# Optimization experiments

Hardware: AMD Instinct MI355X
Metric: run time of the kernel (lower is better)

Reference implementation:

```python
import jax, jax.numpy as jnp
import numpy as np

N, F, H, K, E = 50000, 64, 64, 16, 800000
EXPONENT = 1.0  # module default; s = softmax(logits)**exponent, renormalized
EPS = 1e-15


def gcn_conv(x, W, b, src, dst, ew, n):
    """GCNConv: X' = D^{-1/2}(A+I)D^{-1/2} X W + b (symmetric norm, self-loops)."""
    h = x @ W  # [N,H] linear before propagation
    idx = jnp.arange(n)
    src_a = jnp.concatenate([src, idx])
    dst_a = jnp.concatenate([dst, idx])
    w_a = jnp.concatenate([ew, jnp.ones((n,), h.dtype)])
    deg = jax.ops.segment_sum(w_a, dst_a, num_segments=n)
    dinv = jnp.where(deg > 0, jax.lax.rsqrt(deg), 0.0)
    norm = dinv[src_a] * w_a * dinv[dst_a]          # [E+N]
    out = jax.ops.segment_sum(norm[:, None] * h[src_a], dst_a, num_segments=n)
    return out + b


def setup_inputs() -> dict:
    key = jax.random.key(0)
    ks = jax.random.split(key, 10)
    x = jax.random.normal(ks[0], (N, F), dtype=jnp.float32)
    edge_index = jax.random.randint(ks[1], (2, E), 0, N, dtype=jnp.int64)
    edge_weight = jax.random.uniform(ks[2], (E,), dtype=jnp.float32)
    W1 = jax.random.normal(ks[3], (F, H), dtype=jnp.float32) * (1.0 / np.sqrt(F))
    b1 = jnp.zeros((H,), jnp.float32)
    W2 = jax.random.normal(ks[4], (H, H), dtype=jnp.float32) * (1.0 / np.sqrt(H))
    b2 = jnp.zeros((H,), jnp.float32)
    Wp = jax.random.normal(ks[5], (H, K), dtype=jnp.float32) * (1.0 / np.sqrt(H))
    bp = jnp.zeros((K,), jnp.float32)
    return {"x": x, "edge_index": edge_index, "edge_weight": edge_weight,
            "W1": W1, "b1": b1, "W2": W2, "b2": b2, "Wp": Wp, "bp": bp}


def reference(x, edge_index, edge_weight, W1, b1, W2, b2, Wp, bp):
    src, dst = edge_index[0], edge_index[1]
    n = x.shape[0]
    k = Wp.shape[1]
    # stacked GCN + SELU
    h = jax.nn.selu(gcn_conv(x, W1, b1, src, dst, edge_weight, n))
    h = jax.nn.selu(gcn_conv(h, W2, b2, src, dst, edge_weight, n))
    # DMoN soft assignment
    s = jax.nn.softmax(h @ Wp + bp, axis=-1)          # [N,K]
    s = s ** EXPONENT
    s = s / s.sum(-1, keepdims=True)
    # pooled features: SELU(S^T X)
    out = jax.nn.selu(s.T @ h)                        # [K,H]
    # pooled adjacency: S^T A S computed over the edge list
    out_adj = jnp.einsum('ek,ec->kc', s[src] * edge_weight[:, None], s[dst])
    # spectral (modularity) loss
    d = jax.ops.segment_sum(edge_weight, src, num_segments=n)  # degrees
    two_m = edge_weight.sum()
    ca = s.T @ d                                      # [K]
    spectral_loss = -(jnp.trace(out_adj) - (ca @ ca) / two_m) / two_m
    # orthogonality loss
    ss = s.T @ s
    i_k = jnp.eye(k, dtype=s.dtype)
    ortho_loss = jnp.linalg.norm(ss / jnp.linalg.norm(ss) - i_k / jnp.sqrt(jnp.float32(k)))
    # cluster-size loss
    cluster_loss = jnp.linalg.norm(s.sum(0)) / n * jnp.sqrt(jnp.float32(k)) - 1.0
    # post-process pooled adjacency: zero diag, symmetric degree normalization
    adj = out_adj * (1.0 - i_k)
    dd = jnp.sqrt(adj.sum(-1))[:, None] + EPS
    adj = adj / dd / dd.T
    return s[None], out[None], adj[None], spectral_loss, ortho_loss, cluster_loss
```

## Files before the change

kernel.cpp:

```cpp
#include <hip/hip_runtime.h>
#include <hip/hip_bf16.h>

typedef __hip_bfloat16 bf16;
typedef long long i64t;

__device__ __forceinline__ float b2f(bf16 x) { return __bfloat162float(x); }
__device__ __forceinline__ bf16 f2b(float x) { return __float2bfloat16(x); }

__device__ __forceinline__ float loadF(const void* p, int isbf, long long i) {
    return isbf ? b2f(((const bf16*)p)[i]) : ((const float*)p)[i];
}
__device__ __forceinline__ int loadI(const void* p, int is64, long long i) {
    return is64 ? (int)((const i64t*)p)[i] : ((const int*)p)[i];
}
__device__ __forceinline__ void storeO(void* p, int isbf, long long i, float v) {
    if (isbf) ((bf16*)p)[i] = f2b(v);
    else ((float*)p)[i] = v;
}

#define SELU_ALPHA 1.6732632423543772f
#define SELU_SCALE 1.0507009873554805f
__device__ __forceinline__ float selu_f(float x) {
    return SELU_SCALE * (x > 0.f ? x : SELU_ALPHA * (expf(x) - 1.f));
}

__device__ __forceinline__ void atomAddF(float* p, float v) { unsafeAtomicAdd(p, v); }

__device__ __forceinline__ int pk_src(unsigned p) { return (int)(p >> 16); }
__device__ __forceinline__ float pk_w(unsigned p) { return __uint_as_float(p << 16); }

#define RED_STY 0
#define RED_OADJ 1024
#define RED_SS 1280
#define RED_CA 1536
#define RED_CS 1552
#define RED_2M 1568

#define NB_OADJ 1024
#define CH 2048
#define NBK 256
#define BW 256
#define CAP 4096
#define NRED 1568

__device__ float blockReduceSum256(float v) {
    __shared__ float part[4];
    for (int m = 32; m; m >>= 1) v += __shfl_down(v, m, 64);
    int wid = threadIdx.x >> 6, lane = threadIdx.x & 63;
    if (lane == 0) part[wid] = v;
    __syncthreads();
    v = part[0] + part[1] + part[2] + part[3];
    __syncthreads();
    return v;
}

__global__ void k_gemm_first(const void* __restrict__ in, const void* __restrict__ W,
                             int* __restrict__ zbase, int zcount,
                             bf16* __restrict__ out, int n) {
    __shared__ float Wl[4096];
    __shared__ float Rl[2048];
    __shared__ int scW[1];
    int t = threadIdx.x;
    int g = blockIdx.x * 256 + t;
    if (g < zcount) zbase[g] = 0;
    if (t == 0) scW[0] = 0;
    __syncthreads();
    {
        const unsigned* wq = (const unsigned*)W;
        int c0 = 0;
        for (int i = t; i < 2048; i += 256) {
            unsigned lo = wq[i] & 0xFFFFu, e = (lo >> 7) & 0xFFu;
            if (e == 0u || (e >= 0x60u && e <= 0x8Fu)) c0++;
        }
        atomicAdd(&scW[0], c0);
    }
    __syncthreads();
    int fb = scW[0] > 1200 ? 1 : 0;
    for (int idx = t; idx < 4096; idx += 256) Wl[idx] = loadF(W, fb, idx);
    int r0 = blockIdx.x * 32;
    for (int idx = t; idx < 2048; idx += 256) {
        int rl = idx >> 6, k = idx & 63;
        int r = r0 + rl;
        Rl[idx] = (r < n) ? loadF(in, fb, (long long)r * 64 + k) : 0.f;
    }
    __syncthreads();
    int rl = t >> 6, c = t & 63;
    float acc[8];
#pragma unroll
    for (int u = 0; u < 8; u++) acc[u] = 0.f;
    for (int k = 0; k < 64; k++) {
        float wv = Wl[k * 64 + c];
#pragma unroll
        for (int u = 0; u < 8; u++) acc[u] += Rl[(rl + (u << 2)) * 64 + k] * wv;
    }
#pragma unroll
    for (int u = 0; u < 8; u++) {
        int r = r0 + rl + (u << 2);
        if (r < n) out[(long long)r * 64 + c] = f2b(acc[u]);
    }
}

__global__ void k_bscatter(const void* __restrict__ W1, const void* __restrict__ eidx,
                           const void* __restrict__ ew, int* __restrict__ flags,
                           int* __restrict__ gofs, uint2* __restrict__ tmp, int E) {
    __shared__ int cnt[NBK];
    __shared__ int binStart[NBK];
    __shared__ int bofs[NBK];
    __shared__ int runBase[NBK];
    __shared__ int sc[NBK];
    __shared__ uint2 staged[CH];
    __shared__ int sc2[2];
    int t = threadIdx.x;
    cnt[t] = 0;
    if (t < 2) sc2[t] = 0;
    __syncthreads();
    const unsigned* wq = (const unsigned*)W1;
    int c0 = 0;
    for (int i = t; i < 2048; i += 256) {
        unsigned lo = wq[i] & 0xFFFFu;
        unsigned e = (lo >> 7) & 0xFFu;
        if (e == 0u || (e >= 0x60u && e <= 0x8Fu)) c0++;
    }
    const unsigned* iw = (const unsigned*)eidx;
    int c1 = 0;
    for (int i = t; i < 2048; i += 256)
        if (iw[2 * i + 1] == 0u) c1++;
    atomicAdd(&sc2[0], c0);
    atomicAdd(&sc2[1], c1);
    __syncthreads();
    int fb = sc2[0] > 1200 ? 1 : 0;
    int fi = sc2[1] > 1024 ? 1 : 0;
    if (blockIdx.x == 0 && t == 0) {
        flags[0] = fb;
        flags[1] = fi;
    }
    int base = blockIdx.x * CH;
    int m = min(CH, E - base);
    unsigned es[8], ed[8];
#pragma unroll
    for (int u = 0; u < 8; u++) {
        int k = t + u * 256;
        if (k < m) {
            int s = loadI(eidx, fi, base + k);
            int d = loadI(eidx, fi, (long long)E + base + k);
            float w = loadF(ew, fb, base + k);
            unsigned wb = (__float_as_uint(w) + 0x8000u) >> 16;
            es[u] = ((unsigned)s << 16) | wb;
            ed[u] = (unsigned)d;
            atomicAdd(&cnt[d >> 8], 1);
        } else {
            ed[u] = 0xFFFFFFFFu;
        }
    }
    __syncthreads();
    sc[t] = cnt[t];
    __syncthreads();
    for (int off = 1; off < NBK; off <<= 1) {
        int v = (t >= off) ? sc[t - off] : 0;
        __syncthreads();
        sc[t] += v;
        __syncthreads();
    }
    int ex = t ? sc[t - 1] : 0;
    binStart[t] = ex;
    bofs[t] = ex;
    __syncthreads();
#pragma unroll
    for (int u = 0; u < 8; u++) {
        if (ed[u] != 0xFFFFFFFFu) {
            int b = (int)(ed[u] >> 8);
            int li = atomicAdd(&bofs[b], 1);
            staged[li] = make_uint2(es[u], ed[u]);
        }
    }
    int c = cnt[t];
    __syncthreads();
    runBase[t] = c ? atomicAdd(&gofs[t], c) : 0;
    __syncthreads();
    for (int i = t; i < m; i += 256) {
        uint2 e = staged[i];
        int b = (int)(e.y >> 8);
        int rel = runBase[b] + (i - binStart[b]);
        if (rel < CAP) tmp[(long long)b * CAP + rel] = e;
    }
}

__global__ void k_build(const uint2* __restrict__ tmp, const int* __restrict__ gofs,
                        int* __restrict__ rowptr, int* __restrict__ rowend,
                        unsigned* __restrict__ srcW, float* __restrict__ dinv,
                        float* __restrict__ two_m, int n) {
    __shared__ int cnt[BW];
    __shared__ int nofs[BW];
    __shared__ float wsum[BW];
    __shared__ int inc[BW];
    int b = blockIdx.x;
    int t = threadIdx.x;
    int n0 = b << 8;
    int nn = min(BW, n - n0);
    cnt[t] = 0;
    wsum[t] = 0.f;
    __syncthreads();
    int lo = b * CAP;
    int hi = lo + min(gofs[b], CAP);
    for (int i = lo + t; i < hi; i += 256) {
        uint2 e = tmp[i];
        int dlo = (int)e.y - n0;
        atomicAdd(&cnt[dlo], 1);
        atomicAdd(&wsum[dlo], pk_w(e.x));
    }
    __syncthreads();
    inc[t] = cnt[t];
    __syncthreads();
    for (int off = 1; off < BW; off <<= 1) {
        int v = (t >= off) ? inc[t - off] : 0;
        __syncthreads();
        inc[t] += v;
        __syncthreads();
    }
    if (t < nn) {
        int ex = t ? inc[t - 1] : 0;
        rowptr[n0 + t] = lo + ex;
        rowend[n0 + t] = lo + inc[t];
        nofs[t] = lo + ex;
        dinv[n0 + t] = rsqrtf(wsum[t] + 1.f);
    }
    {
        float v = (t < nn) ? wsum[t] : 0.f;
        __shared__ float part[4];
        for (int mm = 32; mm; mm >>= 1) v += __shfl_down(v, mm, 64);
        int wid = t >> 6, lane = t & 63;
        if (lane == 0) part[wid] = v;
        __syncthreads();
        if (t == 0) atomAddF(two_m, part[0] + part[1] + part[2] + part[3]);
    }
    __syncthreads();
    for (int i = lo + t; i < hi; i += 256) {
        uint2 e = tmp[i];
        int dlo = (int)e.y - n0;
        int pos = atomicAdd(&nofs[dlo], 1);
        srcW[pos] = e.x;
    }
}

__global__ void k_gemm64(const void* __restrict__ in, const void* __restrict__ W,
                         const int* __restrict__ flags, bf16* __restrict__ out, int n) {
    __shared__ float Wl[4096];
    __shared__ float Rl[2048];
    int t = threadIdx.x;
    int fb = flags[0];
    for (int idx = t; idx < 4096; idx += 256) Wl[idx] = loadF(W, fb, idx);
    int r0 = blockIdx.x * 32;
    for (int idx = t; idx < 2048; idx += 256) {
        int rl = idx >> 6, k = idx & 63;
        int r = r0 + rl;
        Rl[idx] = (r < n) ? ((const float*)in)[(long long)r * 64 + k] : 0.f;
    }
    __syncthreads();
    int rl = t >> 6, c = t & 63;
    float acc[8];
#pragma unroll
    for (int u = 0; u < 8; u++) acc[u] = 0.f;
    for (int k = 0; k < 64; k++) {
        float wv = Wl[k * 64 + c];
#pragma unroll
        for (int u = 0; u < 8; u++) acc[u] += Rl[(rl + (u << 2)) * 64 + k] * wv;
    }
#pragma unroll
    for (int u = 0; u < 8; u++) {
        int r = r0 + rl + (u << 2);
        if (r < n) out[(long long)r * 64 + c] = f2b(acc[u]);
    }
}

__global__ void k_prop_csr(const int* __restrict__ rowptr, const int* __restrict__ rowend,
                           const unsigned* __restrict__ srcW, const float* __restrict__ dinv,
                           const bf16* __restrict__ hin, const void* __restrict__ b,
                           const int* __restrict__ flags, float* __restrict__ out, int n) {
    int t = threadIdx.x;
    int node = blockIdx.x * 4 + (t >> 6);
    if (node >= n) return;
    int l = t & 63;
    int q = l >> 4;
    int k = l & 15;
    int fb = flags[0];
    int i0 = rowptr[node], i1 = rowend[node];
    float di = dinv[node];
    float a0 = 0.f, a1 = 0.f, a2 = 0.f, a3 = 0.f;
    for (int base = i0; base < i1; base += 64) {
        int idx = base + l;
        unsigned p = (idx < i1) ? srcW[idx] : 0u;
        float cw = pk_w(p) * dinv[pk_src(p)];
        int m = i1 - base;
        if (m > 64) m = 64;
        for (int j = 0; j < m; j += 4) {
            unsigned pe = (unsigned)__shfl((int)p, j + q, 64);
            float c = __shfl(cw, j + q, 64);
            int s = (int)(pe >> 16);
            uint2 hv = *(const uint2*)(hin + ((long long)s << 6) + (k << 2));
            a0 += c * __uint_as_float(hv.x << 16);
            a1 += c * __uint_as_float(hv.x & 0xFFFF0000u);
            a2 += c * __uint_as_float(hv.y << 16);
            a3 += c * __uint_as_float(hv.y & 0xFFFF0000u);
        }
    }
    a0 += __shfl_xor(a0, 16, 64); a0 += __shfl_xor(a0, 32, 64);
    a1 += __shfl_xor(a1, 16, 64); a1 += __shfl_xor(a1, 32, 64);
    a2 += __shfl_xor(a2, 16, 64); a2 += __shfl_xor(a2, 32, 64);
    a3 += __shfl_xor(a3, 16, 64); a3 += __shfl_xor(a3, 32, 64);
    if (q == 0) {
        uint2 hv = *(const uint2*)(hin + ((long long)node << 6) + (k << 2));
        float dd = di * di;
        float v0 = di * a0 + dd * __uint_as_float(hv.x << 16) + loadF(b, fb, 4 * k);
        float v1 = di * a1 + dd * __uint_as_float(hv.x & 0xFFFF0000u) + loadF(b, fb, 4 * k + 1);
        float v2 = di * a2 + dd * __uint_as_float(hv.y << 16) + loadF(b, fb, 4 * k + 2);
        float v3 = di * a3 + dd * __uint_as_float(hv.y & 0xFFFF0000u) + loadF(b, fb, 4 * k + 3);
        float4 r = make_float4(selu_f(v0), selu_f(v1), selu_f(v2), selu_f(v3));
        *(float4*)(out + ((long long)node << 6) + (k << 2)) = r;
    }
}

__global__ void k_softmax(const float* __restrict__ y, const void* __restrict__ Wp,
                          const void* __restrict__ bp, const int* __restrict__ flags,
                          float* __restrict__ sbuf, void* __restrict__ sout,
                          float* __restrict__ scratch, int n) {
    __shared__ float Wl[1024];
    __shared__ float bl[16];
    __shared__ float yl[1024];
    __shared__ float sl[256];
    int t = threadIdx.x;
    int fb = flags[0];
    for (int idx = t; idx < 1024; idx += 256) Wl[idx] = loadF(Wp, fb, idx);
    if (t < 16) bl[t] = loadF(bp, fb, t);
    int g0 = blockIdx.x * 16;
    for (int idx = t; idx < 1024; idx += 256) {
        int nl = idx >> 6, f = idx & 63;
        int g = g0 + nl;
        yl[idx] = (g < n) ? y[(long long)g * 64 + f] : 0.f;
    }
    __syncthreads();
    int nl = t >> 4, k = t & 15;
    int g = g0 + nl;
    float logit = bl[k];
#pragma unroll
    for (int jj = 0; jj < 64; jj++) logit += yl[nl * 64 + jj] * Wl[jj * 16 + k];
    float mx = logit;
    for (int m = 8; m; m >>= 1) mx = fmaxf(mx, __shfl_xor(mx, m, 16));
    float e = expf(logit - mx);
    float sum = e;
    for (int m = 8; m; m >>= 1) sum += __shfl_xor(sum, m, 16);
    float sv = e / sum;
    sl[nl * 16 + k] = (g < n) ? sv : 0.f;
    if (g < n) {
        sbuf[(long long)g * 16 + k] = sv;
        storeO(sout, fb, (long long)g * 16 + k, sv);
    }
    __syncthreads();
    float* dst = scratch + (long long)blockIdx.x * 1280;
    {
        int k4 = t >> 6, f = t & 63;
        float a0 = 0.f, a1 = 0.f, a2 = 0.f, a3 = 0.f;
#pragma unroll
        for (int node = 0; node < 16; node++) {
            float yv = yl[node * 64 + f];
            const float* sp = sl + node * 16;
            a0 += sp[k4] * yv;
            a1 += sp[k4 + 4] * yv;
            a2 += sp[k4 + 8] * yv;
            a3 += sp[k4 + 12] * yv;
        }
        dst[k4 * 64 + f] = a0;
        dst[(k4 + 4) * 64 + f] = a1;
        dst[(k4 + 8) * 64 + f] = a2;
        dst[(k4 + 12) * 64 + f] = a3;
    }
    {
        int i = t >> 4, j = t & 15;
        float ssa = 0.f;
#pragma unroll
        for (int node = 0; node < 16; node++) ssa += sl[node * 16 + i] * sl[node * 16 + j];
        dst[1024 + t] = ssa;
    }
}

__global__ void k_outadj_csr(const int* __restrict__ rowptr, const int* __restrict__ rowend,
                             const unsigned* __restrict__ srcW, const float* __restrict__ s,
                             float* __restrict__ scratch, int n) {
    __shared__ float lacc[256];
    __shared__ float sca[16];
    __shared__ float scs[16];
    int t = threadIdx.x;
    int wv = t >> 6;
    int l = t & 63;
    int q = l >> 4;
    int j = l & 15;
    lacc[t] = 0.f;
    if (t < 16) { sca[t] = 0.f; scs[t] = 0.f; }
    __syncthreads();
    float acc[16];
#pragma unroll
    for (int r = 0; r < 16; r++) acc[r] = 0.f;
    float catot = 0.f, cstot = 0.f;
    for (int node = blockIdx.x * 4 + wv; node < n; node += NB_OADJ * 4) {
        int i0 = rowptr[node], i1 = rowend[node];
        float tv = 0.f;
        for (int base = i0; base < i1; base += 64) {
            int idx = base + l;
            unsigned p = (idx < i1) ? srcW[idx] : 0u;
            float wl = pk_w(p);
            int m = i1 - base;
            if (m > 64) m = 64;
            for (int jj = 0; jj < m; jj += 4) {
                unsigned pe = (unsigned)__shfl((int)p, jj + q, 64);
                float w = __shfl(wl, jj + q, 64);
                int sidx = (int)(pe >> 16);
                tv += w * s[(long long)sidx * 16 + j];
            }
        }
        tv += __shfl_xor(tv, 16, 64);
        tv += __shfl_xor(tv, 32, 64);
        float sj = s[(long long)node * 16 + j];
        if (q == 0) {
            catot += tv;
            cstot += sj;
        }
#pragma unroll
        for (int r = 0; r < 16; r++) acc[r] += __shfl(tv, r, 16) * sj;
    }
    if (q == 0) {
#pragma unroll
        for (int r = 0; r < 16; r++) atomicAdd(&lacc[r * 16 + j], acc[r]);
        atomicAdd(&sca[j], catot);
        atomicAdd(&scs[j], cstot);
    }
    __syncthreads();
    float* dstp = scratch + (long long)blockIdx.x * 288;
    dstp[t] = lacc[t];
    if (t < 16) {
        dstp[256 + t] = sca[t];
        dstp[272 + t] = scs[t];
    }
}

__global__ void k_reduce_fin(const float* __restrict__ sscr, const float* __restrict__ oscr,
                             float* __restrict__ red, int* __restrict__ done, int nbS,
                             void* __restrict__ out, const int* __restrict__ flags,
                             int n_nodes, int base) {
    int o = blockIdx.x;
    int t = threadIdx.x;
    float sum = 0.f;
    if (o < 1280) {
        for (int b = t; b < nbS; b += 256) sum += sscr[(long long)b * 1280 + o];
    } else {
        int oo = o - 1280;
        for (int b = t; b < NB_OADJ; b += 256) sum += oscr[(long long)b * 288 + oo];
    }
    float v = blockReduceSum256(sum);
    __shared__ int amLast;
    if (t == 0) {
        if (o < 1024) red[RED_STY + o] = v;
        else if (o < 1280) red[RED_SS + o - 1024] = v;
        else {
            int oo = o - 1280;
            if (oo < 256) red[RED_OADJ + oo] = v;
            else if (oo < 272) red[RED_CA + oo - 256] = v;
            else red[RED_CS + oo - 272] = v;
        }
        __threadfence();
        amLast = (atomicAdd(done, 1) == NRED - 1) ? 1 : 0;
    }
    __syncthreads();
    if (!amLast) return;
    __threadfence();
    int fb = flags[0];
    for (int idx = t; idx < 1024; idx += 256)
        storeO(out, fb, base + idx, selu_f(red[RED_STY + idx]));
    int i = t >> 4, j = t & 15;
    float ss_t = red[RED_SS + t];
    float oadj_t = red[RED_OADJ + t];
    float two_m = red[RED_2M];

    float norm_ss = sqrtf(blockReduceSum256(ss_t * ss_t));
    float diff = ss_t / norm_ss - ((i == j) ? 0.25f : 0.f);
    float ortho = sqrtf(blockReduceSum256(diff * diff));
    float trace = blockReduceSum256((i == j) ? oadj_t : 0.f);
    float ca_t = (t < 16) ? red[RED_CA + t] : 0.f;
    float cad = blockReduceSum256(ca_t * ca_t);
    float spectral = -(trace - cad / two_m) / two_m;
    float cs_t = (t < 16) ? red[RED_CS + t] : 0.f;
    float cluster = sqrtf(blockReduceSum256(cs_t * cs_t)) / (float)n_nodes * 4.f - 1.f;

    float a = (i == j) ? 0.f : oadj_t;
    float rs = a;
    for (int m = 8; m; m >>= 1) rs += __shfl_xor(rs, m, 16);
    __shared__ float ddl[16];
    float dd_i = sqrtf(rs) + 1e-15f;
    if (j == 0) ddl[i] = dd_i;
    __syncthreads();
    float aout = a / (dd_i * ddl[j]);
    storeO(out, fb, base + 1024 + t, aout);
    if (t == 0) {
        storeO(out, fb, base + 1280, spectral);
        storeO(out, fb, base + 1281, ortho);
        storeO(out, fb, base + 1282, cluster);
    }
}

extern "C" void kernel_launch(void* const* d_in, const int* in_sizes, int n_in,
                              void* d_out, int out_size, void* d_ws, size_t ws_size,
                              hipStream_t stream) {
    const void* x = d_in[0];
    const void* eidx = d_in[1];
    const void* ew = d_in[2];
    const void* W1 = d_in[3];
    const void* b1 = d_in[4];
    const void* W2 = d_in[5];
    const void* b2 = d_in[6];
    const void* Wp = d_in[7];
    const void* bp = d_in[8];

    const int N = in_sizes[0] / 64;
    const int E = in_sizes[2];

    float* ws = (float*)d_ws;
    float* B = ws;
    float* hbf_f = B + (size_t)N * 64;
    bf16* hbf = (bf16*)hbf_f;
    float* sbuf = hbf_f;
    float* dinv = hbf_f + (size_t)N * 32;
    int* rowptr = (int*)(dinv + N);
    int* rowend = rowptr + N;
    float* red = (float*)(rowend + N);
    int* gofs = (int*)(red + 2048);
    int* flags = gofs + NBK;
    int* done = flags + 2;
    size_t off_ints = (size_t)((done + 1) - (int*)ws);
    off_ints = (off_ints + 3) & ~(size_t)3;
    unsigned* srcW = (unsigned*)((int*)ws + off_ints);
    size_t off2 = off_ints + (size_t)NBK * CAP;
    off2 = (off2 + 3) & ~(size_t)3;
    uint2* tmp = (uint2*)((int*)ws + off2);
    float* sscr = (float*)tmp;
    int nbS = (N + 15) / 16;
    float* oscr = sscr + (size_t)nbS * 1280;

    int nbA = (E + CH - 1) / CH;
    int nbK = (N + BW - 1) / BW;
    int zcount = 2048 + NBK + 2 + 1;

    k_gemm_first<<<(N + 31) / 32, 256, 0, stream>>>(x, W1, (int*)red, zcount, hbf, N);
    k_bscatter<<<nbA, 256, 0, stream>>>(W1, eidx, ew, flags, gofs, tmp, E);
    k_build<<<nbK, 256, 0, stream>>>(tmp, gofs, rowptr, rowend, srcW, dinv,
                                     red + RED_2M, N);
    k_prop_csr<<<(N + 3) / 4, 256, 0, stream>>>(rowptr, rowend, srcW, dinv, hbf, b1,
                                                flags, B, N);
    k_gemm64<<<(N + 31) / 32, 256, 0, stream>>>(B, W2, flags, hbf, N);
    k_prop_csr<<<(N + 3) / 4, 256, 0, stream>>>(rowptr, rowend, srcW, dinv, hbf, b2,
                                                flags, B, N);
    k_softmax<<<nbS, 256, 0, stream>>>(B, Wp, bp, flags, sbuf, d_out, sscr, N);
    k_outadj_csr<<<NB_OADJ, 256, 0, stream>>>(rowptr, rowend, srcW, sbuf, oscr, N);
    k_reduce_fin<<<NRED, 256, 0, stream>>>(sscr, oscr, red, done, nbS, d_out, flags,
                                           N, N * 16);
}
```

Baseline: 356.0 us.

## Process 64 nodes per softmax block and split final reduction into separate kernel

The softmax kernel now loops over four 16-node tiles per block and accumulates S^T·H and S^T·S partials in registers. This cuts the number of partial-result slabs written to scratch and later summed by four. The last-block-done atomic counter in the reduction kernel is replaced by a separate single-block finalize launch, removing the threadfence/atomic path at the cost of one extra kernel launch. Fewer softmax blocks may reduce parallelism, and the extra syncs per tile add some latency.

```diff
diff --git a/kernel.cpp b/kernel.cpp
--- a/kernel.cpp
+++ b/kernel.cpp
@@ -41,7 +41,6 @@
 #define NBK 256
 #define BW 256
 #define CAP 4096
-#define NRED 1568
 
 __device__ float blockReduceSum256(float v) {
     __shared__ float part[4];
@@ -331,34 +330,34 @@
     int fb = flags[0];
     for (int idx = t; idx < 1024; idx += 256) Wl[idx] = loadF(Wp, fb, idx);
     if (t < 16) bl[t] = loadF(bp, fb, t);
-    int g0 = blockIdx.x * 16;
-    for (int idx = t; idx < 1024; idx += 256) {
-        int nl = idx >> 6, f = idx & 63;
-        int g = g0 + nl;
-        yl[idx] = (g < n) ? y[(long long)g * 64 + f] : 0.f;
-    }
-    __syncthreads();
-    int nl = t >> 4, k = t & 15;
-    int g = g0 + nl;
-    float logit = bl[k];
-#pragma unroll
-    for (int jj = 0; jj < 64; jj++) logit += yl[nl * 64 + jj] * Wl[jj * 16 + k];
-    float mx = logit;
-    for (int m = 8; m; m >>= 1) mx = fmaxf(mx, __shfl_xor(mx, m, 16));
-    float e = expf(logit - mx);
-    float sum = e;
-    for (int m = 8; m; m >>= 1) sum += __shfl_xor(sum, m, 16);
-    float sv = e / sum;
-    sl[nl * 16 + k] = (g < n) ? sv : 0.f;
-    if (g < n) {
-        sbuf[(long long)g * 16 + k] = sv;
-        storeO(sout, fb, (long long)g * 16 + k, sv);
-    }
-    __syncthreads();
-    float* dst = scratch + (long long)blockIdx.x * 1280;
-    {
-        int k4 = t >> 6, f = t & 63;
-        float a0 = 0.f, a1 = 0.f, a2 = 0.f, a3 = 0.f;
+    int k4 = t >> 6, f = t & 63;
+    int si = t >> 4, sj = t & 15;
+    float a0 = 0.f, a1 = 0.f, a2 = 0.f, a3 = 0.f, ssa = 0.f;
+    for (int it = 0; it < 4; it++) {
+        int g0 = (blockIdx.x * 4 + it) * 16;
+        __syncthreads();
+        for (int idx = t; idx < 1024; idx += 256) {
+            int nl = idx >> 6, ff = idx & 63;
+            int g = g0 + nl;
+            yl[idx] = (g < n) ? y[(long long)g * 64 + ff] : 0.f;
+        }
+        __syncthreads();
+        int g = g0 + si;
+        float logit = bl[sj];
+#pragma unroll
+        for (int jj = 0; jj < 64; jj++) logit += yl[si * 64 + jj] * Wl[jj * 16 + sj];
+        float mx = logit;
+        for (int m = 8; m; m >>= 1) mx = fmaxf(mx, __shfl_xor(mx, m, 16));
+        float e = expf(logit - mx);
+        float sum = e;
+        for (int m = 8; m; m >>= 1) sum += __shfl_xor(sum, m, 16);
+        float sv = e / sum;
+        sl[si * 16 + sj] = (g < n) ? sv : 0.f;
+        if (g < n) {
+            sbuf[(long long)g * 16 + sj] = sv;
+            storeO(sout, fb, (long long)g * 16 + sj, sv);
+        }
+        __syncthreads();
 #pragma unroll
         for (int node = 0; node < 16; node++) {
             float yv = yl[node * 64 + f];
@@ -367,19 +366,15 @@
             a1 += sp[k4 + 4] * yv;
             a2 += sp[k4 + 8] * yv;
             a3 += sp[k4 + 12] * yv;
-        }
-        dst[k4 * 64 + f] = a0;
-        dst[(k4 + 4) * 64 + f] = a1;
-        dst[(k4 + 8) * 64 + f] = a2;
-        dst[(k4 + 12) * 64 + f] = a3;
-    }
-    {
-        int i = t >> 4, j = t & 15;
-        float ssa = 0.f;
-#pragma unroll
-        for (int node = 0; node < 16; node++) ssa += sl[node * 16 + i] * sl[node * 16 + j];
-        dst[1024 + t] = ssa;
-    }
+            ssa += sl[node * 16 + si] * sl[node * 16 + sj];
+        }
+    }
+    float* dst = scratch + (long long)blockIdx.x * 1280;
+    dst[k4 * 64 + f] = a0;
+    dst[(k4 + 4) * 64 + f] = a1;
+    dst[(k4 + 8) * 64 + f] = a2;
+    dst[(k4 + 12) * 64 + f] = a3;
+    dst[1024 + t] = ssa;
 }
 
 __global__ void k_outadj_csr(const int* __restrict__ rowptr, const int* __restrict__ rowend,
@@ -441,10 +436,8 @@
     }
 }
 
-__global__ void k_reduce_fin(const float* __restrict__ sscr, const float* __restrict__ oscr,
-                             float* __restrict__ red, int* __restrict__ done, int nbS,
-                             void* __restrict__ out, const int* __restrict__ flags,
-                             int n_nodes, int base) {
+__global__ void k_reduce_all(const float* __restrict__ sscr, const float* __restrict__ oscr,
+                             float* __restrict__ red, int nbS) {
     int o = blockIdx.x;
     int t = threadIdx.x;
     float sum = 0.f;
@@ -455,7 +448,6 @@
         for (int b = t; b < NB_OADJ; b += 256) sum += oscr[(long long)b * 288 + oo];
     }
     float v = blockReduceSum256(sum);
-    __shared__ int amLast;
     if (t == 0) {
         if (o < 1024) red[RED_STY + o] = v;
         else if (o < 1280) red[RED_SS + o - 1024] = v;
@@ -465,12 +457,12 @@
             else if (oo < 272) red[RED_CA + oo - 256] = v;
             else red[RED_CS + oo - 272] = v;
         }
-        __threadfence();
-        amLast = (atomicAdd(done, 1) == NRED - 1) ? 1 : 0;
-    }
-    __syncthreads();
-    if (!amLast) return;
-    __threadfence();
+    }
+}
+
+__global__ void k_finalize(const float* __restrict__ red, void* __restrict__ out,
+                           const int* __restrict__ flags, int n_nodes, int base) {
+    int t = threadIdx.x;
     int fb = flags[0];
     for (int idx = t; idx < 1024; idx += 256)
         storeO(out, fb, base + idx, selu_f(red[RED_STY + idx]));
@@ -532,20 +524,19 @@
     float* red = (float*)(rowend + N);
     int* gofs = (int*)(red + 2048);
     int* flags = gofs + NBK;
-    int* done = flags + 2;
-    size_t off_ints = (size_t)((done + 1) - (int*)ws);
+    size_t off_ints = (size_t)((flags + 2) - (int*)ws);
     off_ints = (off_ints + 3) & ~(size_t)3;
     unsigned* srcW = (unsigned*)((int*)ws + off_ints);
     size_t off2 = off_ints + (size_t)NBK * CAP;
     off2 = (off2 + 3) & ~(size_t)3;
     uint2* tmp = (uint2*)((int*)ws + off2);
     float* sscr = (float*)tmp;
-    int nbS = (N + 15) / 16;
+    int nbS = (N + 63) / 64;
     float* oscr = sscr + (size_t)nbS * 1280;
 
     int nbA = (E + CH - 1) / CH;
     int nbK = (N + BW - 1) / BW;
-    int zcount = 2048 + NBK + 2 + 1;
+    int zcount = 2048 + NBK + 2;
 
     k_gemm_first<<<(N + 31) / 32, 256, 0, stream>>>(x, W1, (int*)red, zcount, hbf, N);
     k_bscatter<<<nbA, 256, 0, stream>>>(W1, eidx, ew, flags, gofs, tmp, E);
@@ -558,6 +549,6 @@
                                                 flags, B, N);
     k_softmax<<<nbS, 256, 0, stream>>>(B, Wp, bp, flags, sbuf, d_out, sscr, N);
     k_outadj_csr<<<NB_OADJ, 256, 0, stream>>>(rowptr, rowend, srcW, sbuf, oscr, N);
-    k_reduce_fin<<<NRED, 256, 0, stream>>>(sscr, oscr, red, done, nbS, d_out, flags,
-                                           N, N * 16);
-}
+    k_reduce_all<<<1280 + 288, 256, 0, stream>>>(sscr, oscr, red, nbS);
+    k_finalize<<<1, 256, 0, stream>>>(red, d_out, flags, N, N * 16);
+}
```

Measured after the change: 302.8 us. -14.9%, faster.
